# Kernel tuning notes

Hardware: AMD Instinct MI355X
Metric: run time of the kernel (lower is better)

The kernel has to match this reference:

```python
import jax, jax.numpy as jnp
import numpy as np

WIN = 20  # patch_project window_size
HID = 128


def _lstm_layer(x, w_ih, w_hh, b_ih, b_hh):
    """x: [B,T,D] -> (outputs [B,T,H], final h [B,H]). PyTorch gate order i,f,g,o."""
    B = x.shape[0]
    H = w_hh.shape[1]
    # precompute input contribution for all timesteps: [B,T,4H]
    x_pre = jnp.einsum('btd,gd->btg', x, w_ih) + b_ih + b_hh

    def step(carry, xp):
        h, c = carry
        gates = xp + h @ w_hh.T  # [B,4H]
        i, f, g, o = jnp.split(gates, 4, axis=-1)
        i = jax.nn.sigmoid(i)
        f = jax.nn.sigmoid(f)
        g = jnp.tanh(g)
        o = jax.nn.sigmoid(o)
        c = f * c + i * g
        h = o * jnp.tanh(c)
        return (h, c), h

    h0 = jnp.zeros((B, H), x.dtype)
    c0 = jnp.zeros((B, H), x.dtype)
    (h_f, _), ys = jax.lax.scan(step, (h0, c0), x_pre.transpose(1, 0, 2))
    return ys.transpose(1, 0, 2), h_f


def setup_inputs() -> dict:
    key = jax.random.key(0)
    ks = jax.random.split(key, 20)
    B, S, C = 64, 2048, 32
    D_in = WIN * C          # 640
    D_p = D_in // 2         # 320
    H = HID
    label_len = 48
    s = 0.02
    inp = {
        'inputs': jax.random.normal(ks[0], (B, S, C), jnp.float32),
        '_x': jnp.zeros((B, 4), jnp.float32),
        'y': jnp.zeros((B, label_len), jnp.float32),
        '_y': jnp.zeros((B, 4), jnp.float32),
        'proj_w': jax.random.normal(ks[1], (D_p, D_in), jnp.float32) * s,
        'proj_b': jax.random.normal(ks[2], (D_p,), jnp.float32) * s,
        'w_ih0': jax.random.normal(ks[3], (4 * H, D_p), jnp.float32) * s,
        'w_hh0': jax.random.normal(ks[4], (4 * H, H), jnp.float32) * s,
        'b_ih0': jax.random.normal(ks[5], (4 * H,), jnp.float32) * s,
        'b_hh0': jax.random.normal(ks[6], (4 * H,), jnp.float32) * s,
        'w_ih_rest': jax.random.normal(ks[7], (3, 4 * H, H), jnp.float32) * s,
        'w_hh_rest': jax.random.normal(ks[8], (3, 4 * H, H), jnp.float32) * s,
        'b_ih_rest': jax.random.normal(ks[9], (3, 4 * H), jnp.float32) * s,
        'b_hh_rest': jax.random.normal(ks[10], (3, 4 * H), jnp.float32) * s,
        'out_w': jax.random.normal(ks[11], (label_len, H), jnp.float32) * s,
        'out_b': jax.random.normal(ks[12], (label_len,), jnp.float32) * s,
    }
    return inp


def reference(inputs, _x, y, _y, proj_w, proj_b, w_ih0, w_hh0, b_ih0, b_hh0,
              w_ih_rest, w_hh_rest, b_ih_rest, b_hh_rest, out_w, out_b):
    B, S, C = inputs.shape
    L_out = S - WIN
    idx = jnp.arange(L_out)[:, None] + jnp.arange(WIN)[None, :]
    windows = inputs[:, idx, :].reshape(B, L_out, WIN * C)
    # projection1 (dropout is inference no-op)
    x = jnp.einsum('btd,pd->btp', windows, proj_w) + proj_b
    # 4-layer LSTM (dropout between layers is inference no-op)
    x, h = _lstm_layer(x, w_ih0, w_hh0, b_ih0, b_hh0)
    for l in range(3):
        x, h = _lstm_layer(x, w_ih_rest[l], w_hh_rest[l], b_ih_rest[l], b_hh_rest[l])
    # final hidden state of last layer -> [B,1,H] -> output layer -> [B,1,label_len]
    out = h[:, None, :] @ out_w.T + out_b
    return out
```

## Files before the change

kernel.cpp:

```cpp
#include <hip/hip_runtime.h>
#include <stdint.h>
#include <stddef.h>

typedef __bf16 bf16_t;
typedef bf16_t bf16x8 __attribute__((ext_vector_type(8)));
typedef bf16_t bf16x4 __attribute__((ext_vector_type(4)));
typedef float  f32x4  __attribute__((ext_vector_type(4)));

#define T_STEPS 2028
#define SEQ     2048
#define CIN     32
#define NG      32
#define MB      2
#define CH      32
#define NCH     64
#define RING    4

#define OFF_EFFW   0u
#define OFF_BIAS   655360u
#define OFF_WHH    663552u
#define OFF_WIH    1187840u
#define OFF_CNT    1613824u
#define OFF_XRING  1638400u
#define OFF_YRING  35192832u

__device__ __forceinline__ int endk(int k) {
  int e = (k + 1) * CH;
  return e > T_STEPS ? T_STEPS : e;
}

__device__ __forceinline__ void spin_ge(uint32_t* p, uint32_t tgt) {
  while (atomicAdd(p, 0u) < tgt) __builtin_amdgcn_s_sleep(2);
}
__device__ __forceinline__ void publish(uint32_t* p, uint32_t v) {
  __builtin_amdgcn_fence(__ATOMIC_RELEASE, "agent");
  atomicMax(p, v);
}

__device__ __forceinline__ float fsigm(float x) {
  return __builtin_amdgcn_rcpf(1.0f + __builtin_amdgcn_exp2f(x * -1.44269504089f));
}
__device__ __forceinline__ float ftanh(float x) {
  return 1.0f - 2.0f * __builtin_amdgcn_rcpf(1.0f + __builtin_amdgcn_exp2f(x * 2.88539008178f));
}

__device__ __forceinline__ bf16x8 ldg8(const bf16_t* p) { return *(const bf16x8*)p; }
__device__ __forceinline__ bf16x4 ldg4(const bf16_t* p) { return *(const bf16x4*)p; }

__device__ __forceinline__ bf16x8 ldg_cvt8(const float* p) {
  const f32x4 a = *(const f32x4*)p;
  const f32x4 b = *(const f32x4*)(p + 4);
  bf16x8 r;
  r[0] = (bf16_t)a[0]; r[1] = (bf16_t)a[1]; r[2] = (bf16_t)a[2]; r[3] = (bf16_t)a[3];
  r[4] = (bf16_t)b[0]; r[5] = (bf16_t)b[1]; r[6] = (bf16_t)b[2]; r[7] = (bf16_t)b[3];
  return r;
}


__global__ void k_prep_misc(const float* __restrict__ w_hh0,
                            const float* __restrict__ w_ih_rest,
                            const float* __restrict__ w_hh_rest,
                            const float* __restrict__ b_ih_rest,
                            const float* __restrict__ b_hh_rest,
                            uint8_t* __restrict__ ws) {
  const int bid = blockIdx.x;
  const int l = bid >> 9;
  const int p = bid & 511;
  const int orig = (p & 3) * 128 + (p >> 2);
  const int tid = threadIdx.x;
  bf16_t* whh = (bf16_t*)(ws + OFF_WHH);
  bf16_t* wih = (bf16_t*)(ws + OFF_WIH);
  float* bias = (float*)(ws + OFF_BIAS);
  const float* src = (l == 0) ? (w_hh0 + orig * 128)
                              : (w_hh_rest + ((size_t)(l - 1) * 512 + orig) * 128);
  whh[((size_t)l * 512 + p) * 128 + tid] = (bf16_t)src[tid];
  if (l < 3)
    wih[((size_t)l * 512 + p) * 128 + tid] = (bf16_t)w_ih_rest[((size_t)l * 512 + orig) * 128 + tid];
  if (l >= 1 && tid == 0)
    bias[l * 512 + p] = b_ih_rest[(l - 1) * 512 + orig] + b_hh_rest[(l - 1) * 512 + orig];
  if (bid == 0) {
    uint32_t* cnt = (uint32_t*)(ws + OFF_CNT);
    for (int i = tid; i < 12 * 32 * 16; i += 128) cnt[i] = 0;
  }
}

__global__ void k_prep_effw(const float* __restrict__ proj_w,
                            const float* __restrict__ proj_b,
                            const float* __restrict__ w_ih0,
                            const float* __restrict__ b_ih0,
                            const float* __restrict__ b_hh0,
                            uint8_t* __restrict__ ws) {
  __shared__ float wr[320];
  const int p = blockIdx.x;
  const int orig = (p & 3) * 128 + (p >> 2);
  const int tid = threadIdx.x;
  for (int i = tid; i < 320; i += 256) wr[i] = w_ih0[(size_t)orig * 320 + i];
  __syncthreads();
  bf16_t* effw = (bf16_t*)(ws + OFF_EFFW);
  for (int kk = tid; kk < 640; kk += 256) {
    float a = 0.f;
    for (int z = 0; z < 320; ++z) a += wr[z] * proj_w[(size_t)z * 640 + kk];
    effw[(size_t)p * 640 + kk] = (bf16_t)a;
  }
  if (tid == 0) {
    float a = 0.f;
    for (int z = 0; z < 320; ++z) a += wr[z] * proj_b[z];
    ((float*)(ws + OFF_BIAS))[p] = a + b_ih0[orig] + b_hh0[orig];
  }
}

__global__ __launch_bounds__(256, 1) void k_pipeline(const float* __restrict__ in,
                                                     const float* __restrict__ out_w,
                                                     const float* __restrict__ out_b,
                                                     float* __restrict__ out,
                                                     uint8_t* __restrict__ ws) {
  __shared__ __align__(16) bf16_t h_lds[2][16][136];
  __shared__ f32x4 gate_buf[4][2][32];
  __shared__ float hfl[2][128];

  const int s = blockIdx.x >> 5;
  const int g = blockIdx.x & 31;
  const int tid = threadIdx.x;
  const int lane = tid & 63;
  const int w = tid >> 6;
  const int q = lane >> 4;
  const int ln = lane & 15;

  uint32_t* cnt = (uint32_t*)(ws + OFF_CNT);
  bf16_t* xring = (bf16_t*)(ws + OFF_XRING);
  bf16_t* yring = (bf16_t*)(ws + OFF_YRING);

  if (s == 0) {
    const bf16_t* effw = (const bf16_t*)(ws + OFF_EFFW);
    uint32_t* my = cnt + (0 * NG + g) * 16;
    uint32_t* guard = cnt + (1 * NG + g) * 16;
    for (int k = 0; k < NCH; ++k) {
      if (tid == 0 && k >= RING) spin_ge(guard, (uint32_t)endk(k - RING));
      __syncthreads();
      const int t0 = k * CH;
      f32x4 acc[4][8];
#pragma unroll
      for (int mt = 0; mt < 4; ++mt)
#pragma unroll
        for (int nt = 0; nt < 8; ++nt) acc[mt][nt] = (f32x4){0.f, 0.f, 0.f, 0.f};
#pragma unroll
      for (int kt = 0; kt < 20; ++kt) {
        bf16x8 bfr[8];
#pragma unroll
        for (int nt = 0; nt < 8; ++nt)
          bfr[nt] = ldg8(effw + (size_t)((w * 8 + nt) * 16 + ln) * 640 + kt * 32 + q * 8);
#pragma unroll
        for (int mt = 0; mt < 4; ++mt) {
          int m = mt * 16 + ln;
          int trel = m >> 1, bb = m & 1;
          int tt = t0 + trel; if (tt > T_STEPS - 1) tt = T_STEPS - 1;
          bf16x8 afr = ldg_cvt8(in + (size_t)((g * MB + bb) * SEQ + tt + kt) * CIN + q * 8);
#pragma unroll
          for (int nt = 0; nt < 8; ++nt)
            acc[mt][nt] = __builtin_amdgcn_mfma_f32_16x16x32_bf16(afr, bfr[nt], acc[mt][nt], 0, 0, 0);
        }
      }
      bf16_t* xs = xring + (size_t)((0 * NG + g) * RING + (k & 3)) * (64 * 512);
#pragma unroll
      for (int mt = 0; mt < 4; ++mt)
#pragma unroll
        for (int nt = 0; nt < 8; ++nt)
#pragma unroll
          for (int r = 0; r < 4; ++r)
            xs[(size_t)(mt * 16 + q * 4 + r) * 512 + (w * 8 + nt) * 16 + ln] = (bf16_t)acc[mt][nt][r];
      __syncthreads();
      if (tid == 0) publish(my, (uint32_t)endk(k));
    }
  } else if (s <= 4) {
    const int l = s - 1;
    const bf16_t* whh = (const bf16_t*)(ws + OFF_WHH) + (size_t)l * 512 * 128;
    bf16x8 wfr[8][4];
#pragma unroll
    for (int mt = 0; mt < 8; ++mt)
#pragma unroll
      for (int kt = 0; kt < 4; ++kt)
        wfr[mt][kt] = ldg8(whh + (size_t)(w * 128 + mt * 16 + ln) * 128 + kt * 32 + q * 8);
    const int b_ep = lane >> 5;
    const int j_loc = lane & 31;
    const int jg = w * 32 + j_loc;
    f32x4 biasq = *(const f32x4*)((const float*)(ws + OFF_BIAS) + l * 512 + 4 * jg);
    float c = 0.f;
    {
      bf16_t* hz = &h_lds[0][0][0];
      for (int i = tid; i < 2 * 16 * 136; i += 256) hz[i] = (bf16_t)0.f;
    }
    __syncthreads();
    uint32_t* my = cnt + ((1 + l) * NG + g) * 16;
    uint32_t* prod = (l == 0) ? (cnt + (0 * NG + g) * 16) : (cnt + ((4 + l) * NG + g) * 16);
    uint32_t* yguard = cnt + ((5 + l) * NG + g) * 16;
    const int ly = (l < 3) ? l : 0;

    for (int k = 0; k < NCH; ++k) {
      const int t0 = k * CH;
      const int tlen = (T_STEPS - t0 < CH) ? (T_STEPS - t0) : CH;
      if (tid == 0) {
        spin_ge(prod, (uint32_t)(t0 + tlen));
        if (l < 3 && k >= RING) spin_ge(yguard, (uint32_t)endk(k - RING));
        __builtin_amdgcn_fence(__ATOMIC_ACQUIRE, "agent");
      }
      __syncthreads();
      const bf16_t* xlane = xring + (size_t)((l * NG + g) * RING + (k & 3)) * (64 * 512)
                            + b_ep * 512 + 4 * jg;
      bf16_t* ylane = yring + (size_t)((ly * NG + g) * RING + (k & 3)) * (64 * 128)
                      + b_ep * 128 + jg;

      if (tlen == CH) {
        for (int half = 0; half < 2; ++half) {
          const int tb = t0 + half * 16;
          bf16x4 xq[16];
#pragma unroll
          for (int t = 0; t < 16; ++t) xq[t] = ldg4(xlane + (size_t)(half * 16 + t) * 1024);
          bf16_t yv[16];
#pragma unroll
          for (int t = 0; t < 16; ++t) {
            const int buf = (tb + t) & 1;
            f32x4 acc[8];
#pragma unroll
            for (int mt = 0; mt < 8; ++mt) acc[mt] = (f32x4){0.f, 0.f, 0.f, 0.f};
#pragma unroll
            for (int kt = 0; kt < 3; ++kt) {
              bf16x8 hk = *(const bf16x8*)&h_lds[buf][ln][kt * 32 + q * 8];
#pragma unroll
              for (int mt = 0; mt < 8; ++mt)
                acc[mt] = __builtin_amdgcn_mfma_f32_16x16x32_bf16(wfr[mt][kt], hk, acc[mt], 0, 0, 0);
            }
            {
              bf16x8 hk3 = *(const bf16x8*)&h_lds[buf][ln][3 * 32 + q * 8];
#pragma unroll
              for (int mt = 0; mt < 8; ++mt) {
                acc[mt] = __builtin_amdgcn_mfma_f32_16x16x32_bf16(wfr[mt][3], hk3, acc[mt], 0, 0, 0);
                if (ln < MB) gate_buf[w][ln][mt * 4 + q] = acc[mt];
              }
            }
            f32x4 gq = gate_buf[w][b_ep][j_loc];
            float gi = fsigm(gq[0] + (float)xq[t][0] + biasq[0]);
            float gf = fsigm(gq[1] + (float)xq[t][1] + biasq[1]);
            float gg = ftanh(gq[2] + (float)xq[t][2] + biasq[2]);
            float go = fsigm(gq[3] + (float)xq[t][3] + biasq[3]);
            c = gf * c + gi * gg;
            float hv = go * ftanh(c);
            h_lds[buf ^ 1][b_ep][jg] = (bf16_t)hv;
            yv[t] = (bf16_t)hv;
            asm volatile("s_waitcnt lgkmcnt(0)\n\ts_barrier" ::: "memory");
          }
          if (l < 3) {
#pragma unroll
            for (int t = 0; t < 16; ++t)
              ylane[(size_t)(half * 16 + t) * 256] = yv[t];
          }
        }
      } else {
        for (int trel = 0; trel < tlen; ++trel) {
          const int t = t0 + trel;
          const int buf = t & 1;
          bf16x4 xqs = ldg4(xlane + (size_t)trel * 1024);
          f32x4 acc[8];
#pragma unroll
          for (int mt = 0; mt < 8; ++mt) acc[mt] = (f32x4){0.f, 0.f, 0.f, 0.f};
#pragma unroll
          for (int kt = 0; kt < 4; ++kt) {
            bf16x8 hk = *(const bf16x8*)&h_lds[buf][ln][kt * 32 + q * 8];
#pragma unroll
            for (int mt = 0; mt < 8; ++mt)
              acc[mt] = __builtin_amdgcn_mfma_f32_16x16x32_bf16(wfr[mt][kt], hk, acc[mt], 0, 0, 0);
          }
          if (ln < MB) {
#pragma unroll
            for (int mt = 0; mt < 8; ++mt)
              gate_buf[w][ln][mt * 4 + q] = acc[mt];
          }
          f32x4 gq = gate_buf[w][b_ep][j_loc];
          float gi = fsigm(gq[0] + (float)xqs[0] + biasq[0]);
          float gf = fsigm(gq[1] + (float)xqs[1] + biasq[1]);
          float gg = ftanh(gq[2] + (float)xqs[2] + biasq[2]);
          float go = fsigm(gq[3] + (float)xqs[3] + biasq[3]);
          c = gf * c + gi * gg;
          float hv = go * ftanh(c);
          h_lds[buf ^ 1][b_ep][jg] = (bf16_t)hv;
          if (l < 3) ylane[(size_t)trel * 256] = (bf16_t)hv;
          if (l == 3 && t == T_STEPS - 1) hfl[b_ep][jg] = hv;
          asm volatile("s_waitcnt lgkmcnt(0)\n\ts_barrier" ::: "memory");
        }
      }
      __syncthreads();
      if (tid == 0) publish(my, (uint32_t)(t0 + tlen));
    }

    if (l == 3) {
      __syncthreads();
      if (tid < 96) {
        const int b_loc = tid / 48, o = tid % 48;
        const float* wrow = out_w + (size_t)o * 128;
        float a = out_b[o];
#pragma unroll 4
        for (int j = 0; j < 128; ++j) a += hfl[b_loc][j] * wrow[j];
        out[(size_t)(g * MB + b_loc) * 48 + o] = a;
      }
    }
  } else {
    const int l = s - 4;
    const bf16_t* wih = (const bf16_t*)(ws + OFF_WIH) + (size_t)(l - 1) * 512 * 128;
    bf16x8 bfr[8][4];
#pragma unroll
    for (int nt = 0; nt < 8; ++nt)
#pragma unroll
      for (int kt = 0; kt < 4; ++kt)
        bfr[nt][kt] = ldg8(wih + (size_t)((w * 8 + nt) * 16 + ln) * 128 + kt * 32 + q * 8);
    uint32_t* my = cnt + ((4 + l) * NG + g) * 16;
    uint32_t* prod = cnt + (l * NG + g) * 16;
    uint32_t* xguard = cnt + ((1 + l) * NG + g) * 16;
    for (int k = 0; k < NCH; ++k) {
      if (tid == 0) {
        spin_ge(prod, (uint32_t)endk(k));
        if (k >= RING) spin_ge(xguard, (uint32_t)endk(k - RING));
        __builtin_amdgcn_fence(__ATOMIC_ACQUIRE, "agent");
      }
      __syncthreads();
      const bf16_t* ys = yring + (size_t)(((l - 1) * NG + g) * RING + (k & 3)) * (64 * 128);
      bf16_t* xs = xring + (size_t)((l * NG + g) * RING + (k & 3)) * (64 * 512);
      bf16x8 afr[4][4];
#pragma unroll
      for (int mt = 0; mt < 4; ++mt)
#pragma unroll
        for (int kt = 0; kt < 4; ++kt)
          afr[mt][kt] = ldg8(ys + (size_t)(mt * 16 + ln) * 128 + kt * 32 + q * 8);
#pragma unroll
      for (int mt = 0; mt < 4; ++mt) {
        f32x4 a8[8];
#pragma unroll
        for (int nt = 0; nt < 8; ++nt) a8[nt] = (f32x4){0.f, 0.f, 0.f, 0.f};
#pragma unroll
        for (int kt = 0; kt < 4; ++kt) {
#pragma unroll
          for (int nt = 0; nt < 8; ++nt)
            a8[nt] = __builtin_amdgcn_mfma_f32_16x16x32_bf16(afr[mt][kt], bfr[nt][kt], a8[nt], 0, 0, 0);
        }
#pragma unroll
        for (int nt = 0; nt < 8; ++nt)
#pragma unroll
          for (int r = 0; r < 4; ++r)
            xs[(size_t)(mt * 16 + q * 4 + r) * 512 + (w * 8 + nt) * 16 + ln] = (bf16_t)a8[nt][r];
      }
      __syncthreads();
      if (tid == 0) publish(my, (uint32_t)endk(k));
    }
  }
}

extern "C" void kernel_launch(void* const* d_in, const int* in_sizes, int n_in,
                              void* d_out, int out_size, void* d_ws, size_t ws_size,
                              hipStream_t stream) {
  (void)in_sizes; (void)n_in; (void)out_size; (void)ws_size;
  const float* inputs    = (const float*)d_in[0];
  const float* proj_w    = (const float*)d_in[4];
  const float* proj_b    = (const float*)d_in[5];
  const float* w_ih0     = (const float*)d_in[6];
  const float* w_hh0     = (const float*)d_in[7];
  const float* b_ih0     = (const float*)d_in[8];
  const float* b_hh0     = (const float*)d_in[9];
  const float* w_ih_rest = (const float*)d_in[10];
  const float* w_hh_rest = (const float*)d_in[11];
  const float* b_ih_rest = (const float*)d_in[12];
  const float* b_hh_rest = (const float*)d_in[13];
  const float* out_w     = (const float*)d_in[14];
  const float* out_b     = (const float*)d_in[15];
  uint8_t* ws = (uint8_t*)d_ws;
  float* out = (float*)d_out;

  k_prep_misc<<<dim3(2048), dim3(128), 0, stream>>>(w_hh0, w_ih_rest, w_hh_rest,
                                                    b_ih_rest, b_hh_rest, ws);
  k_prep_effw<<<dim3(512), dim3(256), 0, stream>>>(proj_w, proj_b, w_ih0, b_ih0, b_hh0, ws);
  k_pipeline<<<dim3(256), dim3(256), 0, stream>>>(inputs, out_w, out_b, out, ws);
}
```

Baseline: 2.736 ms.

## Fuse next-layer input projection into LSTM recurrence blocks, drop projection stage

Each recurrent layer block now also holds the next layer's W_ih in registers. It computes the next layer's input gates directly from the h fragments it already reads from LDS, and writes them into the next layer's x ring, one step behind. This removes the separate projection blocks and the y ring round trip, so the grid shrinks from 256 to 160 blocks. The h buffer is re-laid out in LDS as MFMA-ready fragments. In exchange, the serial recurrent loop does twice the MFMA work per step and needs more registers, which could lengthen the critical path.

```diff
diff --git a/kernel.cpp b/kernel.cpp
--- a/kernel.cpp
+++ b/kernel.cpp
@@ -22,7 +22,6 @@
 #define OFF_WIH    1187840u
 #define OFF_CNT    1613824u
 #define OFF_XRING  1638400u
-#define OFF_YRING  35192832u
 
 __device__ __forceinline__ int endk(int k) {
   int e = (k + 1) * CH;
@@ -55,6 +54,8 @@
   r[4] = (bf16_t)b[0]; r[5] = (bf16_t)b[1]; r[6] = (bf16_t)b[2]; r[7] = (bf16_t)b[3];
   return r;
 }
+
+#define MFMA16(a, b, c) __builtin_amdgcn_mfma_f32_16x16x32_bf16((a), (b), (c), 0, 0, 0)
 
 
 __global__ void k_prep_misc(const float* __restrict__ w_hh0,
@@ -114,7 +115,7 @@
                                                      const float* __restrict__ out_b,
                                                      float* __restrict__ out,
                                                      uint8_t* __restrict__ ws) {
-  __shared__ __align__(16) bf16_t h_lds[2][16][136];
+  __shared__ __align__(16) bf16_t hfrag[2][4][64][8];
   __shared__ f32x4 gate_buf[4][2][32];
   __shared__ float hfl[2][128];
 
@@ -128,7 +129,6 @@
 
   uint32_t* cnt = (uint32_t*)(ws + OFF_CNT);
   bf16_t* xring = (bf16_t*)(ws + OFF_XRING);
-  bf16_t* yring = (bf16_t*)(ws + OFF_YRING);
 
   if (s == 0) {
     const bf16_t* effw = (const bf16_t*)(ws + OFF_EFFW);
@@ -157,7 +157,7 @@
           bf16x8 afr = ldg_cvt8(in + (size_t)((g * MB + bb) * SEQ + tt + kt) * CIN + q * 8);
 #pragma unroll
           for (int nt = 0; nt < 8; ++nt)
-            acc[mt][nt] = __builtin_amdgcn_mfma_f32_16x16x32_bf16(afr, bfr[nt], acc[mt][nt], 0, 0, 0);
+            acc[mt][nt] = MFMA16(afr, bfr[nt], acc[mt][nt]);
         }
       }
       bf16_t* xs = xring + (size_t)((0 * NG + g) * RING + (k & 3)) * (64 * 512);
@@ -171,8 +171,9 @@
       __syncthreads();
       if (tid == 0) publish(my, (uint32_t)endk(k));
     }
-  } else if (s <= 4) {
+  } else {
     const int l = s - 1;
+    const bool has_next = (l < 3);
     const bf16_t* whh = (const bf16_t*)(ws + OFF_WHH) + (size_t)l * 512 * 128;
     bf16x8 wfr[8][4];
 #pragma unroll
@@ -180,61 +181,96 @@
 #pragma unroll
       for (int kt = 0; kt < 4; ++kt)
         wfr[mt][kt] = ldg8(whh + (size_t)(w * 128 + mt * 16 + ln) * 128 + kt * 32 + q * 8);
+    bf16x8 wnx[8][4];
+    if (has_next) {
+      const bf16_t* wih = (const bf16_t*)(ws + OFF_WIH) + (size_t)l * 512 * 128;
+#pragma unroll
+      for (int nt = 0; nt < 8; ++nt)
+#pragma unroll
+        for (int kt = 0; kt < 4; ++kt)
+          wnx[nt][kt] = ldg8(wih + (size_t)((w * 8 + nt) * 16 + ln) * 128 + kt * 32 + q * 8);
+    }
     const int b_ep = lane >> 5;
     const int j_loc = lane & 31;
     const int jg = w * 32 + j_loc;
     f32x4 biasq = *(const f32x4*)((const float*)(ws + OFF_BIAS) + l * 512 + 4 * jg);
     float c = 0.f;
     {
-      bf16_t* hz = &h_lds[0][0][0];
-      for (int i = tid; i < 2 * 16 * 136; i += 256) hz[i] = (bf16_t)0.f;
+      bf16_t* hz = &hfrag[0][0][0][0];
+      for (int i = tid; i < 2 * 4 * 64 * 8; i += 256) hz[i] = (bf16_t)0.f;
     }
     __syncthreads();
     uint32_t* my = cnt + ((1 + l) * NG + g) * 16;
-    uint32_t* prod = (l == 0) ? (cnt + (0 * NG + g) * 16) : (cnt + ((4 + l) * NG + g) * 16);
-    uint32_t* yguard = cnt + ((5 + l) * NG + g) * 16;
-    const int ly = (l < 3) ? l : 0;
+    uint32_t* prod = cnt + (l * NG + g) * 16;
+    uint32_t* xguard = cnt + ((2 + l) * NG + g) * 16;
+
+    bf16_t* hwr0 = &hfrag[0][w][(j_loc >> 3) * 16 + b_ep][j_loc & 7];
+    bf16_t* hwr1 = &hfrag[1][w][(j_loc >> 3) * 16 + b_ep][j_loc & 7];
+    const bf16_t* hrd0 = &hfrag[0][0][lane][0];
+    const bf16_t* hrd1 = &hfrag[1][0][lane][0];
 
     for (int k = 0; k < NCH; ++k) {
       const int t0 = k * CH;
       const int tlen = (T_STEPS - t0 < CH) ? (T_STEPS - t0) : CH;
       if (tid == 0) {
         spin_ge(prod, (uint32_t)(t0 + tlen));
-        if (l < 3 && k >= RING) spin_ge(yguard, (uint32_t)endk(k - RING));
+        if (has_next && k >= RING) spin_ge(xguard, (uint32_t)endk(k - RING));
         __builtin_amdgcn_fence(__ATOMIC_ACQUIRE, "agent");
       }
       __syncthreads();
       const bf16_t* xlane = xring + (size_t)((l * NG + g) * RING + (k & 3)) * (64 * 512)
                             + b_ep * 512 + 4 * jg;
-      bf16_t* ylane = yring + (size_t)((ly * NG + g) * RING + (k & 3)) * (64 * 128)
-                      + b_ep * 128 + jg;
+      bf16_t* xout = xring + (size_t)(((has_next ? l + 1 : l) * NG + g) * RING + (k & 3)) * (64 * 512)
+                     + ln * 512 + w * 128;
 
       if (tlen == CH) {
         for (int half = 0; half < 2; ++half) {
-          const int tb = t0 + half * 16;
           bf16x4 xq[16];
 #pragma unroll
           for (int t = 0; t < 16; ++t) xq[t] = ldg4(xlane + (size_t)(half * 16 + t) * 1024);
-          bf16_t yv[16];
 #pragma unroll
           for (int t = 0; t < 16; ++t) {
-            const int buf = (tb + t) & 1;
+            const int buf = t & 1;
+            const bf16_t* hr = buf ? hrd1 : hrd0;
+            bf16x8 hk0 = *(const bf16x8*)(hr);
+            bf16x8 hk1 = *(const bf16x8*)(hr + 512);
+            bf16x8 hk2 = *(const bf16x8*)(hr + 1024);
+            bf16x8 hk3 = *(const bf16x8*)(hr + 1536);
             f32x4 acc[8];
 #pragma unroll
             for (int mt = 0; mt < 8; ++mt) acc[mt] = (f32x4){0.f, 0.f, 0.f, 0.f};
 #pragma unroll
-            for (int kt = 0; kt < 3; ++kt) {
-              bf16x8 hk = *(const bf16x8*)&h_lds[buf][ln][kt * 32 + q * 8];
-#pragma unroll
-              for (int mt = 0; mt < 8; ++mt)
-                acc[mt] = __builtin_amdgcn_mfma_f32_16x16x32_bf16(wfr[mt][kt], hk, acc[mt], 0, 0, 0);
+            for (int mt = 0; mt < 8; ++mt) acc[mt] = MFMA16(wfr[mt][0], hk0, acc[mt]);
+#pragma unroll
+            for (int mt = 0; mt < 8; ++mt) acc[mt] = MFMA16(wfr[mt][1], hk1, acc[mt]);
+#pragma unroll
+            for (int mt = 0; mt < 8; ++mt) acc[mt] = MFMA16(wfr[mt][2], hk2, acc[mt]);
+#pragma unroll
+            for (int mt = 0; mt < 8; ++mt) acc[mt] = MFMA16(wfr[mt][3], hk3, acc[mt]);
+            if (ln < MB) {
+#pragma unroll
+              for (int mt = 0; mt < 8; ++mt) gate_buf[w][ln][mt * 4 + q] = acc[mt];
             }
-            {
-              bf16x8 hk3 = *(const bf16x8*)&h_lds[buf][ln][3 * 32 + q * 8];
-#pragma unroll
-              for (int mt = 0; mt < 8; ++mt) {
-                acc[mt] = __builtin_amdgcn_mfma_f32_16x16x32_bf16(wfr[mt][3], hk3, acc[mt], 0, 0, 0);
-                if (ln < MB) gate_buf[w][ln][mt * 4 + q] = acc[mt];
+            if (has_next && (half + t)) {
+              f32x4 a2[8];
+#pragma unroll
+              for (int nt = 0; nt < 8; ++nt) a2[nt] = (f32x4){0.f, 0.f, 0.f, 0.f};
+#pragma unroll
+              for (int nt = 0; nt < 8; ++nt) a2[nt] = MFMA16(wnx[nt][0], hk0, a2[nt]);
+#pragma unroll
+              for (int nt = 0; nt < 8; ++nt) a2[nt] = MFMA16(wnx[nt][1], hk1, a2[nt]);
+#pragma unroll
+              for (int nt = 0; nt < 8; ++nt) a2[nt] = MFMA16(wnx[nt][2], hk2, a2[nt]);
+#pragma unroll
+              for (int nt = 0; nt < 8; ++nt) a2[nt] = MFMA16(wnx[nt][3], hk3, a2[nt]);
+              if (ln < MB) {
+#pragma unroll
+                for (int nt = 0; nt < 8; ++nt) {
+                  bf16x4 v;
+                  v[0] = (bf16_t)a2[nt][0]; v[1] = (bf16_t)a2[nt][1];
+                  v[2] = (bf16_t)a2[nt][2]; v[3] = (bf16_t)a2[nt][3];
+                  *(bf16x4*)(xout + (size_t)(half * 16 + t - 1) * 1024 + nt * 16 + q * 4) = v;
+                }
               }
             }
             f32x4 gq = gate_buf[w][b_ep][j_loc];
@@ -244,35 +280,56 @@
             float go = fsigm(gq[3] + (float)xq[t][3] + biasq[3]);
             c = gf * c + gi * gg;
             float hv = go * ftanh(c);
-            h_lds[buf ^ 1][b_ep][jg] = (bf16_t)hv;
-            yv[t] = (bf16_t)hv;
+            *(buf ? hwr0 : hwr1) = (bf16_t)hv;
             asm volatile("s_waitcnt lgkmcnt(0)\n\ts_barrier" ::: "memory");
-          }
-          if (l < 3) {
-#pragma unroll
-            for (int t = 0; t < 16; ++t)
-              ylane[(size_t)(half * 16 + t) * 256] = yv[t];
           }
         }
       } else {
         for (int trel = 0; trel < tlen; ++trel) {
           const int t = t0 + trel;
-          const int buf = t & 1;
+          const int buf = trel & 1;
+          const bf16_t* hr = buf ? hrd1 : hrd0;
           bf16x4 xqs = ldg4(xlane + (size_t)trel * 1024);
+          bf16x8 hk0 = *(const bf16x8*)(hr);
+          bf16x8 hk1 = *(const bf16x8*)(hr + 512);
+          bf16x8 hk2 = *(const bf16x8*)(hr + 1024);
+          bf16x8 hk3 = *(const bf16x8*)(hr + 1536);
           f32x4 acc[8];
 #pragma unroll
           for (int mt = 0; mt < 8; ++mt) acc[mt] = (f32x4){0.f, 0.f, 0.f, 0.f};
 #pragma unroll
-          for (int kt = 0; kt < 4; ++kt) {
-            bf16x8 hk = *(const bf16x8*)&h_lds[buf][ln][kt * 32 + q * 8];
-#pragma unroll
-            for (int mt = 0; mt < 8; ++mt)
-              acc[mt] = __builtin_amdgcn_mfma_f32_16x16x32_bf16(wfr[mt][kt], hk, acc[mt], 0, 0, 0);
+          for (int mt = 0; mt < 8; ++mt) acc[mt] = MFMA16(wfr[mt][0], hk0, acc[mt]);
+#pragma unroll
+          for (int mt = 0; mt < 8; ++mt) acc[mt] = MFMA16(wfr[mt][1], hk1, acc[mt]);
+#pragma unroll
+          for (int mt = 0; mt < 8; ++mt) acc[mt] = MFMA16(wfr[mt][2], hk2, acc[mt]);
+#pragma unroll
+          for (int mt = 0; mt < 8; ++mt) acc[mt] = MFMA16(wfr[mt][3], hk3, acc[mt]);
+          if (ln < MB) {
+#pragma unroll
+            for (int mt = 0; mt < 8; ++mt) gate_buf[w][ln][mt * 4 + q] = acc[mt];
           }
-          if (ln < MB) {
-#pragma unroll
-            for (int mt = 0; mt < 8; ++mt)
-              gate_buf[w][ln][mt * 4 + q] = acc[mt];
+          if (has_next && trel) {
+            f32x4 a2[8];
+#pragma unroll
+            for (int nt = 0; nt < 8; ++nt) a2[nt] = (f32x4){0.f, 0.f, 0.f, 0.f};
+#pragma unroll
+            for (int nt = 0; nt < 8; ++nt) a2[nt] = MFMA16(wnx[nt][0], hk0, a2[nt]);
+#pragma unroll
+            for (int nt = 0; nt < 8; ++nt) a2[nt] = MFMA16(wnx[nt][1], hk1, a2[nt]);
+#pragma unroll
+            for (int nt = 0; nt < 8; ++nt) a2[nt] = MFMA16(wnx[nt][2], hk2, a2[nt]);
+#pragma unroll
+            for (int nt = 0; nt < 8; ++nt) a2[nt] = MFMA16(wnx[nt][3], hk3, a2[nt]);
+            if (ln < MB) {
+#pragma unroll
+              for (int nt = 0; nt < 8; ++nt) {
+                bf16x4 v;
+                v[0] = (bf16_t)a2[nt][0]; v[1] = (bf16_t)a2[nt][1];
+                v[2] = (bf16_t)a2[nt][2]; v[3] = (bf16_t)a2[nt][3];
+                *(bf16x4*)(xout + (size_t)(trel - 1) * 1024 + nt * 16 + q * 4) = v;
+              }
+            }
           }
           f32x4 gq = gate_buf[w][b_ep][j_loc];
           float gi = fsigm(gq[0] + (float)xqs[0] + biasq[0]);
@@ -281,10 +338,34 @@
           float go = fsigm(gq[3] + (float)xqs[3] + biasq[3]);
           c = gf * c + gi * gg;
           float hv = go * ftanh(c);
-          h_lds[buf ^ 1][b_ep][jg] = (bf16_t)hv;
-          if (l < 3) ylane[(size_t)trel * 256] = (bf16_t)hv;
+          *(buf ? hwr0 : hwr1) = (bf16_t)hv;
           if (l == 3 && t == T_STEPS - 1) hfl[b_ep][jg] = hv;
           asm volatile("s_waitcnt lgkmcnt(0)\n\ts_barrier" ::: "memory");
+        }
+      }
+      if (has_next) {
+        bf16x8 f0 = *(const bf16x8*)(hrd0);
+        bf16x8 f1 = *(const bf16x8*)(hrd0 + 512);
+        bf16x8 f2 = *(const bf16x8*)(hrd0 + 1024);
+        bf16x8 f3 = *(const bf16x8*)(hrd0 + 1536);
+        f32x4 a2[8];
+#pragma unroll
+        for (int nt = 0; nt < 8; ++nt) a2[nt] = (f32x4){0.f, 0.f, 0.f, 0.f};
+#pragma unroll
+        for (int nt = 0; nt < 8; ++nt) {
+          a2[nt] = MFMA16(wnx[nt][0], f0, a2[nt]);
+          a2[nt] = MFMA16(wnx[nt][1], f1, a2[nt]);
+          a2[nt] = MFMA16(wnx[nt][2], f2, a2[nt]);
+          a2[nt] = MFMA16(wnx[nt][3], f3, a2[nt]);
+        }
+        if (ln < MB) {
+#pragma unroll
+          for (int nt = 0; nt < 8; ++nt) {
+            bf16x4 v;
+            v[0] = (bf16_t)a2[nt][0]; v[1] = (bf16_t)a2[nt][1];
+            v[2] = (bf16_t)a2[nt][2]; v[3] = (bf16_t)a2[nt][3];
+            *(bf16x4*)(xout + (size_t)(tlen - 1) * 1024 + nt * 16 + q * 4) = v;
+          }
         }
       }
       __syncthreads();
@@ -301,53 +382,6 @@
         for (int j = 0; j < 128; ++j) a += hfl[b_loc][j] * wrow[j];
         out[(size_t)(g * MB + b_loc) * 48 + o] = a;
       }
-    }
-  } else {
-    const int l = s - 4;
-    const bf16_t* wih = (const bf16_t*)(ws + OFF_WIH) + (size_t)(l - 1) * 512 * 128;
-    bf16x8 bfr[8][4];
-#pragma unroll
-    for (int nt = 0; nt < 8; ++nt)
-#pragma unroll
-      for (int kt = 0; kt < 4; ++kt)
-        bfr[nt][kt] = ldg8(wih + (size_t)((w * 8 + nt) * 16 + ln) * 128 + kt * 32 + q * 8);
-    uint32_t* my = cnt + ((4 + l) * NG + g) * 16;
-    uint32_t* prod = cnt + (l * NG + g) * 16;
-    uint32_t* xguard = cnt + ((1 + l) * NG + g) * 16;
-    for (int k = 0; k < NCH; ++k) {
-      if (tid == 0) {
-        spin_ge(prod, (uint32_t)endk(k));
-        if (k >= RING) spin_ge(xguard, (uint32_t)endk(k - RING));
-        __builtin_amdgcn_fence(__ATOMIC_ACQUIRE, "agent");
-      }
-      __syncthreads();
-      const bf16_t* ys = yring + (size_t)(((l - 1) * NG + g) * RING + (k & 3)) * (64 * 128);
-      bf16_t* xs = xring + (size_t)((l * NG + g) * RING + (k & 3)) * (64 * 512);
-      bf16x8 afr[4][4];
-#pragma unroll
-      for (int mt = 0; mt < 4; ++mt)
-#pragma unroll
-        for (int kt = 0; kt < 4; ++kt)
-          afr[mt][kt] = ldg8(ys + (size_t)(mt * 16 + ln) * 128 + kt * 32 + q * 8);
-#pragma unroll
-      for (int mt = 0; mt < 4; ++mt) {
-        f32x4 a8[8];
-#pragma unroll
-        for (int nt = 0; nt < 8; ++nt) a8[nt] = (f32x4){0.f, 0.f, 0.f, 0.f};
-#pragma unroll
-        for (int kt = 0; kt < 4; ++kt) {
-#pragma unroll
-          for (int nt = 0; nt < 8; ++nt)
-            a8[nt] = __builtin_amdgcn_mfma_f32_16x16x32_bf16(afr[mt][kt], bfr[nt][kt], a8[nt], 0, 0, 0);
-        }
-#pragma unroll
-        for (int nt = 0; nt < 8; ++nt)
-#pragma unroll
-          for (int r = 0; r < 4; ++r)
-            xs[(size_t)(mt * 16 + q * 4 + r) * 512 + (w * 8 + nt) * 16 + ln] = (bf16_t)a8[nt][r];
-      }
-      __syncthreads();
-      if (tid == 0) publish(my, (uint32_t)endk(k));
     }
   }
 }
@@ -375,5 +409,5 @@
   k_prep_misc<<<dim3(2048), dim3(128), 0, stream>>>(w_hh0, w_ih_rest, w_hh_rest,
                                                     b_ih_rest, b_hh_rest, ws);
   k_prep_effw<<<dim3(512), dim3(256), 0, stream>>>(proj_w, proj_b, w_ih0, b_ih0, b_hh0, ws);
-  k_pipeline<<<dim3(256), dim3(256), 0, stream>>>(inputs, out_w, out_b, out, ws);
-}
+  k_pipeline<<<dim3(160), dim3(256), 0, stream>>>(inputs, out_w, out_b, out, ws);
+}
```

After: 2.728 ms, median of 2. No clear change (-0.3%).
